# Optimization experiments

Hardware: AMD Instinct MI355X
Metric: run time of the kernel (lower is better)

## Reference

```python
import jax, jax.numpy as jnp
import numpy as np

B = 256        # batch size
D = 256        # d_model
H = 8          # num_heads
DH = 32        # d_head
MAXLEN = 256   # max(lengths)


def setup_inputs() -> dict:
    rng = np.random.default_rng(0)
    lengths = rng.integers(32, MAXLEN + 1, size=B)
    lengths[0] = MAXLEN  # ensure max(lengths) == MAXLEN (static)
    total = int(lengths.sum())
    key = jax.random.key(0)
    ks = jax.random.split(key, 6)
    x = jax.random.normal(ks[0], (total, D), jnp.float32)
    w_scale = 0.05
    Wq = jax.random.normal(ks[1], (D, H * DH), jnp.float32) * w_scale
    Wk = jax.random.normal(ks[2], (D, H * DH), jnp.float32) * w_scale
    Wv = jax.random.normal(ks[3], (D, H * DH), jnp.float32) * w_scale
    Wo = jax.random.normal(ks[4], (H * DH, D), jnp.float32) * w_scale
    cls_emb = jax.random.normal(ks[5], (D,), jnp.float32)
    return dict(x=x, lengths=jnp.asarray(lengths, jnp.int32), max_len=MAXLEN,
                Wq=Wq, Wk=Wk, Wv=Wv, Wo=Wo, cls_emb=cls_emb)


def reference(x, lengths, max_len, Wq, Wk, Wv, Wo, cls_emb):
    Bn = lengths.shape[0]
    total = x.shape[0]
    Lp1 = max_len + 1  # room for CLS token appended at position lengths[i]

    # scatter packed tokens -> padded [B, Lp1, D] (vectorized pad_packed_tensor)
    cum = jnp.cumsum(lengths)
    tok = jnp.arange(total)
    bid = jnp.searchsorted(cum, tok, side='right')       # batch id per token
    pos = tok - (cum[bid] - lengths[bid])                # position within sample
    padded = jnp.zeros((Bn, Lp1, x.shape[1]), x.dtype).at[bid, pos].set(x)
    # place CLS embedding at position lengths[i] of each sample
    padded = padded.at[jnp.arange(Bn), lengths].set(cls_emb.astype(x.dtype))

    q = (padded @ Wq).reshape(Bn, Lp1, H, DH)
    k = (padded @ Wk).reshape(Bn, Lp1, H, DH)
    v = (padded @ Wv).reshape(Bn, Lp1, H, DH)

    e = jnp.einsum('bxhd,byhd->bhxy', q, k) / jnp.asarray(np.sqrt(DH), x.dtype)
    valid = jnp.arange(Lp1)[None, :] <= lengths[:, None]           # [B, Lp1]
    mask = valid[:, None, :, None] & valid[:, None, None, :]       # [B,1,Lp1,Lp1]
    e = jnp.where(mask, e, jnp.asarray(-1e10, e.dtype))
    alpha = jax.nn.softmax(e, axis=-1)

    out = jnp.einsum('bhxy,byhd->bxhd', alpha, v).reshape(Bn, Lp1, H * DH) @ Wo
    # CLS-token gather readout: token at index lengths[i] per sample
    cls = out[jnp.arange(Bn), lengths]  # [B, D]
    return cls, alpha
```

## Files before the change

### kernel.cpp

```cpp
#include <hip/hip_runtime.h>
#include <hip/hip_bf16.h>
#include <math.h>

#define BATCH 256
#define DMODEL 256
#define NHEAD 8
#define DHEAD 32
#define LP1 257
#define CH 5
#define NFILL 2
#define SCALE 0.17677669529663687f


typedef __attribute__((ext_vector_type(8))) _Float16 half8;
typedef __attribute__((ext_vector_type(4))) float floatx4;

__global__ __launch_bounds__(256) void k_scan(const int* __restrict__ lengths,
                                              int* __restrict__ offsets,
                                              int* __restrict__ valid_off) {
    __shared__ int s[BATCH];
    int t = threadIdx.x;
    int v = lengths[t];
    s[t] = v;
    __syncthreads();
    for (int d = 1; d < BATCH; d <<= 1) {
        int add = (t >= d) ? s[t - d] : 0;
        __syncthreads();
        s[t] += add;
        __syncthreads();
    }
    offsets[t]   = s[t] - v;
    valid_off[t] = s[t] - v + t;
}

__global__ __launch_bounds__(256) void k_prep(const float* __restrict__ x,
                                              const float* __restrict__ cls_emb,
                                              const float* __restrict__ Wq,
                                              const float* __restrict__ Wk,
                                              const int* __restrict__ lengths,
                                              const int* __restrict__ valid_off,
                                              int M, int packN,
                                              _Float16* __restrict__ Ah,
                                              _Float16* __restrict__ Wt) {
    int bx = blockIdx.x, t = threadIdx.x;
    if (bx < packN) {
        int row = bx * 8 + (t >> 5);
        int lane32 = t & 31;
        half8 hv = {};
        if (row < M) {
            int lo = 0, hi = 255;
            #pragma unroll
            for (int it = 0; it < 8; ++it) {
                int mid = (lo + hi + 1) >> 1;
                if (valid_off[mid] <= row) lo = mid; else hi = mid - 1;
            }
            int b = lo;
            int p = row - valid_off[b];
            const float* src = (p < lengths[b]) ? (x + (size_t)(row - b) * DMODEL) : cls_emb;
            float4 v0 = *(const float4*)&src[lane32 * 8];
            float4 v1 = *(const float4*)&src[lane32 * 8 + 4];
            hv[0] = (_Float16)v0.x; hv[1] = (_Float16)v0.y; hv[2] = (_Float16)v0.z; hv[3] = (_Float16)v0.w;
            hv[4] = (_Float16)v1.x; hv[5] = (_Float16)v1.y; hv[6] = (_Float16)v1.z; hv[7] = (_Float16)v1.w;
        }
        *(half8*)&Ah[(size_t)row * DMODEL + lane32 * 8] = hv;
    } else {
        int n = (bx - packN) * 8 + (t >> 5);
        int k0 = (t & 31) * 8;
        const float* W = (n < 256) ? Wq : Wk;
        int nc = n & 255;
        half8 hv;
        #pragma unroll
        for (int j = 0; j < 8; ++j) hv[j] = (_Float16)W[(size_t)(k0 + j) * DMODEL + nc];
        *(half8*)&Wt[(size_t)n * DMODEL + k0] = hv;
    }
}

__global__ __launch_bounds__(256) void k_gemm(const _Float16* __restrict__ Ah,
                                              const _Float16* __restrict__ Wt,
                                              int rows_pad,
                                              _Float16* __restrict__ Qh,
                                              _Float16* __restrict__ Kh) {
    __shared__ _Float16 As[128][72];
    __shared__ _Float16 Bs[128][72];
    int t = threadIdx.x;
    int l = t & 63, w = t >> 6;
    int wm = (w >> 1) * 64, wn = (w & 1) * 64;
    int r0 = blockIdx.x * 128;
    int col0 = blockIdx.y * 128;
    int li = l & 15, k0 = (l >> 4) * 8;

    floatx4 acc[4][4] = {};

    for (int kc = 0; kc < 256; kc += 64) {
        #pragma unroll
        for (int jj = 0; jj < 4; ++jj) {
            int idx = t + jj * 256;
            int rl = idx >> 3, q = idx & 7;
            *(half8*)&As[rl][q * 8] = *(const half8*)&Ah[(size_t)(r0 + rl) * DMODEL + kc + q * 8];
            *(half8*)&Bs[rl][q * 8] = *(const half8*)&Wt[(size_t)(col0 + rl) * DMODEL + kc + q * 8];
        }
        __syncthreads();
        half8 a[4][2], bf[4][2];
        #pragma unroll
        for (int m = 0; m < 4; ++m) {
            a[m][0] = *(half8*)&As[wm + m * 16 + li][k0];
            a[m][1] = *(half8*)&As[wm + m * 16 + li][k0 + 32];
        }
        #pragma unroll
        for (int n = 0; n < 4; ++n) {
            bf[n][0] = *(half8*)&Bs[wn + n * 16 + li][k0];
            bf[n][1] = *(half8*)&Bs[wn + n * 16 + li][k0 + 32];
        }
        #pragma unroll
        for (int s = 0; s < 2; ++s)
            #pragma unroll
            for (int m = 0; m < 4; ++m)
                #pragma unroll
                for (int n = 0; n < 4; ++n)
                    acc[m][n] = __builtin_amdgcn_mfma_f32_16x16x32_f16(a[m][s], bf[n][s], acc[m][n], 0, 0, 0);
        __syncthreads();
    }

    int rfrag = (l >> 4) * 4;
    #pragma unroll
    for (int n = 0; n < 4; ++n) {
        int cg = col0 + wn + n * 16 + li;
        _Float16* dst = (cg < 256) ? Qh : Kh;
        size_t hb = (size_t)((cg >> 5) & 7) * rows_pad;
        int cc = cg & 31;
        #pragma unroll
        for (int m = 0; m < 4; ++m) {
            int row = r0 + wm + m * 16 + rfrag;
            #pragma unroll
            for (int f = 0; f < 4; ++f)
                dst[(hb + row + f) * DHEAD + cc] = (_Float16)acc[m][n][f];
        }
    }
}

__global__ __launch_bounds__(256) void k_attn(const _Float16* __restrict__ Qh,
                                              const _Float16* __restrict__ Kh,
                                              const int* __restrict__ lengths,
                                              const int* __restrict__ valid_off,
                                              int rows_pad,
                                              float* __restrict__ alpha) {
    int c = blockIdx.x, b = blockIdx.y, h = blockIdx.z;
    int len  = __builtin_amdgcn_readfirstlane(lengths[b]);
    int base = __builtin_amdgcn_readfirstlane(valid_off[b]);
    int t = threadIdx.x;
    float* out = alpha + (size_t)(b * NHEAD + h) * (size_t)(LP1 * LP1);

    if (c >= CH) {
        if (len >= 256) return;
        const float inv257 = 1.f / 257.f;
        int S = (len + 1) * LP1;
        int E = LP1 * LP1;
        int half = ((E - S) / NFILL) & ~3;
        int fs = S + (c - CH) * half;
        int fe = (c - CH == NFILL - 1) ? E : fs + half;
        int A = (fs + 3) & ~3;
        if (fs + t < A && fs + t < fe) __builtin_nontemporal_store(inv257, &out[fs + t]);
        int B4 = fe & ~3;
        floatx4 v4 = {inv257, inv257, inv257, inv257};
        for (int j = (A >> 2) + t; (j << 2) < B4; j += 256)
            __builtin_nontemporal_store(v4, (floatx4*)&out[j << 2]);
        if (B4 + t < fe) __builtin_nontemporal_store(inv257, &out[B4 + t]);
        return;
    }

    int r0 = c * 64;
    if (r0 > len) return;

    __shared__ _Float16 tile[64 * LP1];

    int l = t & 63;
    int w = t >> 6;
    int rt = r0 + w * 16;
    int li = l & 15, k0 = (l >> 4) * 8;
    bool full = (len == 256);

    if (rt <= len) {
        const _Float16* Qb = Qh + ((size_t)h * rows_pad + base) * DHEAD;
        const _Float16* Kb = Kh + ((size_t)h * rows_pad + base) * DHEAD;

        half8 a = *(const half8*)&Qb[(rt + li) * DHEAD + k0];

        floatx4 acc[16];
        #pragma unroll
        for (int g = 0; g < 2; ++g) {
            half8 bf[8];
            #pragma unroll
            for (int j = 0; j < 8; ++j)
                bf[j] = *(const half8*)&Kb[((g * 8 + j) * 16 + li) * DHEAD + k0];
            #pragma unroll
            for (int j = 0; j < 8; ++j)
                acc[g * 8 + j] = __builtin_amdgcn_mfma_f32_16x16x32_f16(a, bf[j], (floatx4){0.f, 0.f, 0.f, 0.f}, 0, 0, 0);
        }

        float p256[4] = {0.f, 0.f, 0.f, 0.f};
        if (full) {
            half8 b256 = {};
            if (li == 0) b256 = *(const half8*)&Kb[256 * DHEAD + k0];
            floatx4 a256 = __builtin_amdgcn_mfma_f32_16x16x32_f16(a, b256, (floatx4){0.f, 0.f, 0.f, 0.f}, 0, 0, 0);
            #pragma unroll
            for (int f = 0; f < 4; ++f) p256[f] = __expf(a256[f] * SCALE);
        }

        float rowsum[4] = {0.f, 0.f, 0.f, 0.f};
        #pragma unroll
        for (int ct = 0; ct < 16; ++ct) {
            bool cm = (ct * 16 + li) <= len;
            #pragma unroll
            for (int f = 0; f < 4; ++f) {
                float pv = cm ? __expf(acc[ct][f] * SCALE) : 0.f;
                acc[ct][f] = pv;
                rowsum[f] += pv;
            }
        }
        if (full && li == 0) {
            #pragma unroll
            for (int f = 0; f < 4; ++f) rowsum[f] += p256[f];
        }
        #pragma unroll
        for (int off = 1; off < 16; off <<= 1) {
            #pragma unroll
            for (int f = 0; f < 4; ++f) rowsum[f] += __shfl_xor(rowsum[f], off);
        }

        #pragma unroll
        for (int f = 0; f < 4; ++f) {
            int row = rt + (l >> 4) * 4 + f;
            if (row <= len) {
                float inv = 1.f / rowsum[f];
                int lb = (row - r0) * LP1;
                #pragma unroll
                for (int ct = 0; ct < 16; ++ct)
                    tile[lb + ct * 16 + li] = (_Float16)(acc[ct][f] * inv);
                if (li == 0)
                    tile[lb + 256] = (_Float16)(full ? p256[f] * inv : 0.f);
            }
        }
    }
    __syncthreads();

    int rlast = min(len, r0 + 63);
    int cnt = (rlast - r0 + 1) * LP1;
    float* g = out + (size_t)r0 * LP1;
    for (int j = t; j < cnt; j += 256)
        __builtin_nontemporal_store((float)tile[j], &g[j]);
}

__global__ __launch_bounds__(512) void k_out(const float* __restrict__ x,
                                             const float* __restrict__ cls_emb,
                                             const float* __restrict__ Wv,
                                             const float* __restrict__ Wo,
                                             const int* __restrict__ lengths,
                                             const int* __restrict__ offsets,
                                             const float* __restrict__ alpha,
                                             float* __restrict__ cls_out) {
    int b = blockIdx.x, t = threadIdx.x;
    int col = t & 255, grp = t >> 8;
    int len = lengths[b], off = offsets[b];

    __shared__ float aw[LP1][8];
    __shared__ float ctx2[2][NHEAD][DMODEL];
    __shared__ float po[2][DMODEL];
    __shared__ float po2[2][DMODEL];

    int L1 = len + 1;
    for (int i = t; i < L1 * 8; i += 512) {
        int y = i >> 3, h = i & 7;
        aw[y][h] = alpha[((size_t)(b * NHEAD + h) * LP1 + len) * LP1 + y];
    }
    __syncthreads();

    float acc[NHEAD] = {};
    int y0 = grp ? (L1 >> 1) : 0;
    int y1 = grp ? L1 : (L1 >> 1);
    for (int y = y0; y < y1; ++y) {
        float xv = (y < len) ? x[(size_t)(off + y) * DMODEL + col] : cls_emb[col];
        float4 a0 = *(const float4*)&aw[y][0];
        float4 a1 = *(const float4*)&aw[y][4];
        acc[0] += a0.x * xv; acc[1] += a0.y * xv; acc[2] += a0.z * xv; acc[3] += a0.w * xv;
        acc[4] += a1.x * xv; acc[5] += a1.y * xv; acc[6] += a1.z * xv; acc[7] += a1.w * xv;
    }
    #pragma unroll
    for (int h = 0; h < NHEAD; ++h) ctx2[grp][h][col] = acc[h];
    __syncthreads();

    {
        int n = col, h = n >> 5;
        float s = 0.f;
        for (int c = grp * 128; c < grp * 128 + 128; ++c)
            s += (ctx2[0][h][c] + ctx2[1][h][c]) * Wv[(size_t)c * DMODEL + n];
        po[grp][n] = s;
    }
    __syncthreads();

    {
        int n = col;
        float s = 0.f;
        for (int c = grp * 128; c < grp * 128 + 128; ++c)
            s += (po[0][c] + po[1][c]) * Wo[(size_t)c * DMODEL + n];
        po2[grp][n] = s;
    }
    __syncthreads();

    if (grp == 0)
        cls_out[(size_t)b * DMODEL + col] = po2[0][col] + po2[1][col];
}

extern "C" void kernel_launch(void* const* d_in, const int* in_sizes, int n_in,
                              void* d_out, int out_size, void* d_ws, size_t ws_size,
                              hipStream_t stream) {
    const float* x       = (const float*)d_in[0];
    const int*   lengths = (const int*)d_in[1];
    const float* Wq      = (const float*)d_in[3];
    const float* Wk      = (const float*)d_in[4];
    const float* Wv      = (const float*)d_in[5];
    const float* Wo      = (const float*)d_in[6];
    const float* cls_emb = (const float*)d_in[7];

    int total = in_sizes[0] / DMODEL;
    int M = total + BATCH;
    int rows_pad = ((M + 256 + 127) / 128) * 128;

    float* out     = (float*)d_out;
    float* cls_out = out;
    float* alpha   = out + BATCH * DMODEL;

    char* wsb = (char*)d_ws;
    int* offsets   = (int*)wsb;
    int* valid_off = (int*)(wsb + 1024);
    size_t o = 2048;
    _Float16* Ah = (_Float16*)(wsb + o);  o += (size_t)rows_pad * DMODEL * 2;
    o = ((o + 255) / 256) * 256;
    _Float16* Wt = (_Float16*)(wsb + o);  o += (size_t)512 * DMODEL * 2;
    o = ((o + 255) / 256) * 256;
    _Float16* Qh = (_Float16*)(wsb + o);  o += (size_t)rows_pad * DMODEL * 2;
    _Float16* Kh = (_Float16*)(wsb + o);

    int packN = rows_pad / 8;

    k_scan<<<1, 256, 0, stream>>>(lengths, offsets, valid_off);
    k_prep<<<packN + 64, 256, 0, stream>>>(x, cls_emb, Wq, Wk, lengths, valid_off,
                                           M, packN, Ah, Wt);

    dim3 g2(rows_pad / 128, 4);
    k_gemm<<<g2, 256, 0, stream>>>(Ah, Wt, rows_pad, Qh, Kh);

    dim3 g3(CH + NFILL, BATCH, NHEAD);
    k_attn<<<g3, 256, 0, stream>>>(Qh, Kh, lengths, valid_off, rows_pad, alpha);

    k_out<<<BATCH, 512, 0, stream>>>(x, cls_emb, Wv, Wo, lengths, offsets, alpha, cls_out);
}
```

Measured before the change: 270.2 us.

## Fuse length scan into prep kernel and read fp16 packed activations in output stage

Drops the separate single-block scan kernel. Each prep block now recomputes the prefix sum of lengths in shared memory and does its binary search there, and one block writes valid_off to global for later kernels. The output kernel now reads the fp16 padded activation buffer Ah, which already includes the CLS row, instead of fp32 x plus cls_emb, so it loads half the bytes and has no branch. The costs are redundant scan work in every prep block and lower precision in the context accumulation.

```diff
diff --git a/kernel.cpp b/kernel.cpp
--- a/kernel.cpp
+++ b/kernel.cpp
@@ -15,34 +15,34 @@
 typedef __attribute__((ext_vector_type(8))) _Float16 half8;
 typedef __attribute__((ext_vector_type(4))) float floatx4;
 
-__global__ __launch_bounds__(256) void k_scan(const int* __restrict__ lengths,
-                                              int* __restrict__ offsets,
-                                              int* __restrict__ valid_off) {
-    __shared__ int s[BATCH];
-    int t = threadIdx.x;
-    int v = lengths[t];
-    s[t] = v;
-    __syncthreads();
-    for (int d = 1; d < BATCH; d <<= 1) {
-        int add = (t >= d) ? s[t - d] : 0;
-        __syncthreads();
-        s[t] += add;
-        __syncthreads();
-    }
-    offsets[t]   = s[t] - v;
-    valid_off[t] = s[t] - v + t;
-}
-
 __global__ __launch_bounds__(256) void k_prep(const float* __restrict__ x,
                                               const float* __restrict__ cls_emb,
                                               const float* __restrict__ Wq,
                                               const float* __restrict__ Wk,
                                               const int* __restrict__ lengths,
-                                              const int* __restrict__ valid_off,
                                               int M, int packN,
                                               _Float16* __restrict__ Ah,
-                                              _Float16* __restrict__ Wt) {
+                                              _Float16* __restrict__ Wt,
+                                              int* __restrict__ valid_off_g) {
+    __shared__ int vo[BATCH];
+    __shared__ int ln[BATCH];
     int bx = blockIdx.x, t = threadIdx.x;
+
+    int v = lengths[t];
+    ln[t] = v;
+    vo[t] = v;
+    __syncthreads();
+    for (int d = 1; d < BATCH; d <<= 1) {
+        int add = (t >= d) ? vo[t - d] : 0;
+        __syncthreads();
+        vo[t] += add;
+        __syncthreads();
+    }
+    int ivo = vo[t] - v + t;
+    __syncthreads();
+    vo[t] = ivo;
+    __syncthreads();
+
     if (bx < packN) {
         int row = bx * 8 + (t >> 5);
         int lane32 = t & 31;
@@ -52,11 +52,10 @@
             #pragma unroll
             for (int it = 0; it < 8; ++it) {
                 int mid = (lo + hi + 1) >> 1;
-                if (valid_off[mid] <= row) lo = mid; else hi = mid - 1;
+                if (vo[mid] <= row) lo = mid; else hi = mid - 1;
             }
-            int b = lo;
-            int p = row - valid_off[b];
-            const float* src = (p < lengths[b]) ? (x + (size_t)(row - b) * DMODEL) : cls_emb;
+            int p = row - vo[lo];
+            const float* src = (p < ln[lo]) ? (x + (size_t)(row - lo) * DMODEL) : cls_emb;
             float4 v0 = *(const float4*)&src[lane32 * 8];
             float4 v1 = *(const float4*)&src[lane32 * 8 + 4];
             hv[0] = (_Float16)v0.x; hv[1] = (_Float16)v0.y; hv[2] = (_Float16)v0.z; hv[3] = (_Float16)v0.w;
@@ -64,6 +63,7 @@
         }
         *(half8*)&Ah[(size_t)row * DMODEL + lane32 * 8] = hv;
     } else {
+        if (bx == packN) valid_off_g[t] = vo[t];
         int n = (bx - packN) * 8 + (t >> 5);
         int k0 = (t & 31) * 8;
         const float* W = (n < 256) ? Wq : Wk;
@@ -250,17 +250,16 @@
         __builtin_nontemporal_store((float)tile[j], &g[j]);
 }
 
-__global__ __launch_bounds__(512) void k_out(const float* __restrict__ x,
-                                             const float* __restrict__ cls_emb,
+__global__ __launch_bounds__(512) void k_out(const _Float16* __restrict__ Ah,
                                              const float* __restrict__ Wv,
                                              const float* __restrict__ Wo,
                                              const int* __restrict__ lengths,
-                                             const int* __restrict__ offsets,
+                                             const int* __restrict__ valid_off,
                                              const float* __restrict__ alpha,
                                              float* __restrict__ cls_out) {
     int b = blockIdx.x, t = threadIdx.x;
     int col = t & 255, grp = t >> 8;
-    int len = lengths[b], off = offsets[b];
+    int len = lengths[b], base = valid_off[b];
 
     __shared__ float aw[LP1][8];
     __shared__ float ctx2[2][NHEAD][DMODEL];
@@ -278,7 +277,7 @@
     int y0 = grp ? (L1 >> 1) : 0;
     int y1 = grp ? L1 : (L1 >> 1);
     for (int y = y0; y < y1; ++y) {
-        float xv = (y < len) ? x[(size_t)(off + y) * DMODEL + col] : cls_emb[col];
+        float xv = (float)Ah[(size_t)(base + y) * DMODEL + col];
         float4 a0 = *(const float4*)&aw[y][0];
         float4 a1 = *(const float4*)&aw[y][4];
         acc[0] += a0.x * xv; acc[1] += a0.y * xv; acc[2] += a0.z * xv; acc[3] += a0.w * xv;
@@ -330,7 +329,6 @@
     float* alpha   = out + BATCH * DMODEL;
 
     char* wsb = (char*)d_ws;
-    int* offsets   = (int*)wsb;
     int* valid_off = (int*)(wsb + 1024);
     size_t o = 2048;
     _Float16* Ah = (_Float16*)(wsb + o);  o += (size_t)rows_pad * DMODEL * 2;
@@ -342,9 +340,8 @@
 
     int packN = rows_pad / 8;
 
-    k_scan<<<1, 256, 0, stream>>>(lengths, offsets, valid_off);
-    k_prep<<<packN + 64, 256, 0, stream>>>(x, cls_emb, Wq, Wk, lengths, valid_off,
-                                           M, packN, Ah, Wt);
+    k_prep<<<packN + 64, 256, 0, stream>>>(x, cls_emb, Wq, Wk, lengths,
+                                           M, packN, Ah, Wt, valid_off);
 
     dim3 g2(rows_pad / 128, 4);
     k_gemm<<<g2, 256, 0, stream>>>(Ah, Wt, rows_pad, Qh, Kh);
@@ -352,5 +349,5 @@
     dim3 g3(CH + NFILL, BATCH, NHEAD);
     k_attn<<<g3, 256, 0, stream>>>(Qh, Kh, lengths, valid_off, rows_pad, alpha);
 
-    k_out<<<BATCH, 512, 0, stream>>>(x, cls_emb, Wv, Wo, lengths, offsets, alpha, cls_out);
-}
+    k_out<<<BATCH, 512, 0, stream>>>(Ah, Wv, Wo, lengths, valid_off, alpha, cls_out);
+}
```

Measured after the change: 262.2 us. 1.03x faster.
